# Kernel optimization log

Hardware: AMD Instinct MI355X
Metric: run time of the kernel (lower is better)

## Reference

```python
import jax, jax.numpy as jnp
import numpy as np

B, L, D = 8, 4096, 128
TEMPERATURE = 1.0


def setup_inputs() -> dict:
    key = jax.random.key(0)
    kx, kw, kb = jax.random.split(key, 3)
    x = jax.random.normal(kx, (B, L, D), dtype=jnp.float32)
    # nn.Linear(dim, dim): weight [D, D], bias [D]
    bound = 1.0 / np.sqrt(D)
    W = jax.random.uniform(kw, (D, D), minval=-bound, maxval=bound, dtype=jnp.float32)
    b = jax.random.uniform(kb, (D,), minval=-bound, maxval=bound, dtype=jnp.float32)
    return {"x": x, "W": W, "b": b}


def reference(x, W, b):
    # projected = proj(x): torch Linear is x @ W.T + b
    projected = jnp.einsum("bld,ed->ble", x, W) + b            # [B, L, D]

    # adaptive_avg_pool1d over sequence length L -> L//2 (L even => pair means)
    Bq, Lx, Dx = x.shape
    q = x.reshape(Bq, Lx // 2, 2, Dx).mean(axis=2)             # [B, L/2, D]
    q = jnp.einsum("bld,ed->ble", q, W) + b                    # [B, L/2, D]

    # pairwise squared euclidean distance via ||q||^2 + ||k||^2 - 2 q.k (GEMM form)
    q_sq = jnp.sum(q * q, axis=-1, keepdims=True)              # [B, L/2, 1]
    k_sq = jnp.sum(projected * projected, axis=-1)[:, None, :] # [B, 1, L]
    qk = jnp.einsum("bqd,bkd->bqk", q, projected)              # [B, L/2, L]
    power = jnp.maximum(q_sq + k_sq - 2.0 * qk, 0.0)
    distances = jnp.sqrt(power)
    similarities = jnp.exp(-distances * TEMPERATURE)           # [B, L/2, L]

    k = jnp.einsum("bqk,bkd->bqd", similarities, projected)    # [B, L/2, D]
    v = k
    return (q, k, v)
```

## Files before the change

### kernel.cpp

```cpp
#include <hip/hip_runtime.h>
#include <hip/hip_bf16.h>
#include <stdint.h>

#define NB 8
#define LL 4096
#define LQ 2048
#define DD 128

typedef __attribute__((ext_vector_type(8))) short short8;
typedef __attribute__((ext_vector_type(4))) short short4v;
typedef __attribute__((ext_vector_type(4))) float f4;
typedef __attribute__((ext_vector_type(2))) unsigned int u2;

typedef const __attribute__((address_space(1))) unsigned int guint_t;
typedef __attribute__((address_space(3))) unsigned int luint_t;

__device__ __forceinline__ short8 pack8(const float* v) {
    __hip_bfloat16 h[8];
    #pragma unroll
    for (int j = 0; j < 8; ++j) h[j] = __float2bfloat16(v[j]);
    return *(short8*)h;
}

__global__ __launch_bounds__(256) void projA_kernel(
    const float* __restrict__ x, const float* __restrict__ W,
    const float* __restrict__ bias,
    __hip_bfloat16* __restrict__ proj_sw, __hip_bfloat16* __restrict__ projT_sw,
    __hip_bfloat16* __restrict__ qb, float* __restrict__ qf,
    float* __restrict__ psq, float* __restrict__ qsq)
{
    __shared__ __hip_bfloat16 Wlds[128 * 128];
    __shared__ __hip_bfloat16 Tt[4][128 * 16];

    const int tid = threadIdx.x;
    const int lane = tid & 63, w = tid >> 6;
    const int lr = lane & 15, lh = lane >> 4;

    #pragma unroll
    for (int k = 0; k < 16; ++k) {
        const int f = k * 1024 + tid * 4;
        const int e = f >> 7, col = f & 127;
        f4 v = *(const f4*)&W[f];
        __hip_bfloat16 h[4];
        #pragma unroll
        for (int j = 0; j < 4; ++j) h[j] = __float2bfloat16(v[j]);
        const int byte = e * 256 + (((col * 2)) ^ ((e & 7) << 4));
        *(u2*)((char*)Wlds + byte) = *(u2*)h;
    }
    float bv[8];
    #pragma unroll
    for (int nt = 0; nt < 8; ++nt) bv[nt] = bias[nt * 16 + lr];
    __syncthreads();

    const int tile = blockIdx.x;
    const int row0 = tile * 64 + w * 16;
    const bool qmode = tile >= (NB * LL / 64);

    short8 a[4];
    if (!qmode) {
        const float* src = x + (size_t)(row0 + lr) * DD;
        #pragma unroll
        for (int ks = 0; ks < 4; ++ks) {
            float t[8];
            *(f4*)&t[0] = *(const f4*)&src[ks * 32 + lh * 8];
            *(f4*)&t[4] = *(const f4*)&src[ks * 32 + lh * 8 + 4];
            a[ks] = pack8(t);
        }
    } else {
        const int gq = row0 - NB * LL + lr;
        const int b = gq >> 11, l = gq & 2047;
        const float* s0 = x + ((size_t)b * LL + 2 * l) * DD;
        #pragma unroll
        for (int ks = 0; ks < 4; ++ks) {
            float t[8];
            f4 u0 = *(const f4*)&s0[ks * 32 + lh * 8];
            f4 u1 = *(const f4*)&s0[ks * 32 + lh * 8 + 4];
            f4 v0 = *(const f4*)&s0[DD + ks * 32 + lh * 8];
            f4 v1 = *(const f4*)&s0[DD + ks * 32 + lh * 8 + 4];
            *(f4*)&t[0] = (u0 + v0) * 0.5f;
            *(f4*)&t[4] = (u1 + v1) * 0.5f;
            a[ks] = pack8(t);
        }
    }

    f4 acc[8] = {};
    #pragma unroll
    for (int nt = 0; nt < 8; ++nt) {
        const int e = nt * 16 + lr;
        #pragma unroll
        for (int ks = 0; ks < 4; ++ks) {
            const int byte = e * 256 + ((ks * 64 + lh * 16) ^ ((lr & 7) << 4));
            short8 bk = *(const short8*)((char*)Wlds + byte);
            acc[nt] = __builtin_amdgcn_mfma_f32_16x16x32_bf16(a[ks], bk, acc[nt], 0, 0, 0);
        }
    }

    __hip_bfloat16 h[8][4];
    f4 rn = {0.f, 0.f, 0.f, 0.f};
    #pragma unroll
    for (int nt = 0; nt < 8; ++nt)
        #pragma unroll
        for (int r = 0; r < 4; ++r) {
            float v = acc[nt][r] + bv[nt];
            acc[nt][r] = v;
            h[nt][r] = __float2bfloat16(v);
            float vb = __bfloat162float(h[nt][r]);
            rn[r] += vb * vb;
        }
    #pragma unroll
    for (int m = 1; m < 16; m <<= 1) {
        #pragma unroll
        for (int r = 0; r < 4; ++r) rn[r] += __shfl_xor(rn[r], m);
    }

    if (!qmode) {
        const int gr = row0;
        #pragma unroll
        for (int nt = 0; nt < 8; ++nt)
            #pragma unroll
            for (int r = 0; r < 4; ++r) {
                const int row = gr + lh * 4 + r;
                const int byte = (nt * 32 + lr * 2) ^ (((lh * 4 + r) & 7) << 4);
                *(__hip_bfloat16*)((char*)proj_sw + (size_t)row * 256 + byte) =
                    __float2bfloat16(-2.0f * __bfloat162float(h[nt][r]));
            }
        if (lr == 0) *(f4*)&psq[gr + lh * 4] = rn;
        #pragma unroll
        for (int nt = 0; nt < 8; ++nt) {
            __hip_bfloat16 p[4] = {h[nt][0], h[nt][1], h[nt][2], h[nt][3]};
            *(u2*)((char*)&Tt[w][0] + (nt * 16 + lr) * 32 + lh * 8) = *(u2*)p;
        }
        const int b = gr >> 12, l0 = gr & 4095;
        #pragma unroll
        for (int i = 0; i < 2; ++i) {
            const int e = lane + i * 64;
            const int sw = (e & 15) << 3;
            char* rowbase = (char*)projT_sw + ((size_t)(b * DD + e)) * (LL * 2)
                          + (size_t)(l0 & ~63) * 2;
            const int ob = (l0 & 63) * 2;
            #pragma unroll
            for (int c = 0; c < 4; ++c) {
                u2 chunk = *(u2*)((char*)&Tt[w][e * 16] + c * 8);
                *(u2*)(rowbase + ((ob + c * 8) ^ sw)) = chunk;
            }
        }
    } else {
        const int gq = row0 - NB * LL;
        #pragma unroll
        for (int nt = 0; nt < 8; ++nt)
            #pragma unroll
            for (int r = 0; r < 4; ++r) {
                const size_t idx = (size_t)(gq + lh * 4 + r) * DD + nt * 16 + lr;
                qb[idx] = h[nt][r];
                qf[idx] = acc[nt][r];
            }
        if (lr == 0) *(f4*)&qsq[gq + lh * 4] = rn;
    }
}

__global__ __launch_bounds__(1024, 4) void fused_kernel(
    const __hip_bfloat16* __restrict__ proj_sw, const __hip_bfloat16* __restrict__ projT_sw,
    const __hip_bfloat16* __restrict__ qb, const float* __restrict__ psq,
    const float* __restrict__ qsq,
    float* __restrict__ pp0, float* __restrict__ pp1,
    float* __restrict__ pp2, float* __restrict__ pp3, int keys_per)
{
    __shared__ __hip_bfloat16 pbuf[2][8192];
    __shared__ __hip_bfloat16 tbuf[2][8192];
    __shared__ __align__(16) float psbuf[1024];

    const int bid = blockIdx.x;
    const int b = bid & 7;
    const int qt8 = (bid >> 3) & 7;
    const int ks = bid >> 6;
    const int tid = threadIdx.x;
    const int w = tid >> 6, lane = tid & 63;
    const int lr = lane & 15, lh = lane >> 4;

    const int qrow0 = qt8 * 256 + w * 16;
    const int key0 = ks * keys_per;
    const int ntiles = keys_per / 64;

    const char* psw = (const char*)proj_sw + (size_t)b * LL * 256;
    const char* ptbsw = (const char*)projT_sw + (size_t)b * DD * LL * 2;
    const float* psb = psq + b * LL;

    for (int i = tid; i < keys_per; i += 1024) psbuf[i] = psb[key0 + i];

    short8 aq[4];
    const __hip_bfloat16* qbase = qb + ((size_t)b * LQ + qrow0) * DD;
    #pragma unroll
    for (int kss = 0; kss < 4; ++kss)
        aq[kss] = *(const short8*)&qbase[(size_t)lr * DD + kss * 32 + lh * 8];
    const float qn = qsq[b * LQ + qrow0 + lr];

    __syncthreads();

    const char* sp = psw + (size_t)key0 * 256 + w * 1024;
    const char* st = ptbsw + (size_t)(w * 8 + (lane >> 3)) * (LL * 2)
                   + (size_t)key0 * 2 + (lane & 7) * 16;
    auto stage = [&](int buf) {
        __builtin_amdgcn_global_load_lds(
            (guint_t*)(sp + lane * 16),
            (luint_t*)&pbuf[buf][w * 512 + lane * 8], 16, 0, 0);
        __builtin_amdgcn_global_load_lds(
            (guint_t*)st,
            (luint_t*)&tbuf[buf][w * 512 + lane * 8], 16, 0, 0);
        sp += 64 * 256;
        st += 64 * 2;
    };

    stage(0);
    stage(1);

    f4 oc[8] = {};
    int p = 0;

    for (int t = 0; t < ntiles; ++t) {
        if (t + 1 < ntiles) asm volatile("s_waitcnt vmcnt(2)" ::: "memory");
        else                asm volatile("s_waitcnt vmcnt(0)" ::: "memory");
        asm volatile("s_barrier" ::: "memory");

        #pragma unroll
        for (int sub = 0; sub < 2; ++sub) {
            f4 pn0 = *(const f4*)&psbuf[t * 64 + sub * 32 + lh * 4];
            f4 pn1 = *(const f4*)&psbuf[t * 64 + sub * 32 + 16 + lh * 4];
            f4 s0, s1;
            #pragma unroll
            for (int r = 0; r < 4; ++r) {
                s0[r] = qn + pn0[r];
                s1[r] = qn + pn1[r];
            }
            __builtin_amdgcn_s_setprio(1);
            #pragma unroll
            for (int kss = 0; kss < 4; ++kss) {
                const int off = (kss * 64 + lh * 16) ^ ((lr & 7) << 4);
                short8 ak0 = *(const short8*)((const char*)pbuf[p] + (sub * 32 + lr) * 256 + off);
                short8 ak1 = *(const short8*)((const char*)pbuf[p] + (sub * 32 + 16 + lr) * 256 + off);
                s0 = __builtin_amdgcn_mfma_f32_16x16x32_bf16(ak0, aq[kss], s0, 0, 0, 0);
                s1 = __builtin_amdgcn_mfma_f32_16x16x32_bf16(ak1, aq[kss], s1, 0, 0, 0);
            }
            __builtin_amdgcn_s_setprio(0);

            alignas(16) __hip_bfloat16 hh[8];
            #pragma unroll
            for (int r = 0; r < 4; ++r) {
                float d0 = __builtin_amdgcn_sqrtf(fmaxf(s0[r], 0.0f));
                float d1 = __builtin_amdgcn_sqrtf(fmaxf(s1[r], 0.0f));
                hh[r]     = __float2bfloat16(__expf(-d0));
                hh[4 + r] = __float2bfloat16(__expf(-d1));
            }
            const short8 pa = *(short8*)hh;

            __builtin_amdgcn_s_setprio(1);
            #pragma unroll
            for (int dt = 0; dt < 8; ++dt) {
                const char* rowp = (const char*)tbuf[p] + (dt * 16 + lr) * 128;
                const int sw = lr << 3;
                union { short8 v; short4v h[2]; } u;
                u.h[0] = *(const short4v*)(rowp + ((lh * 8 + sub * 64) ^ sw));
                u.h[1] = *(const short4v*)(rowp + ((lh * 8 + 32 + sub * 64) ^ sw));
                oc[dt] = __builtin_amdgcn_mfma_f32_16x16x32_bf16(pa, u.v, oc[dt], 0, 0, 0);
            }
            __builtin_amdgcn_s_setprio(0);
        }

        asm volatile("s_barrier" ::: "memory");
        if (t + 2 < ntiles) stage(p);
        p ^= 1;
    }

    float* pb = (ks == 0) ? pp0 : (ks == 1) ? pp1 : (ks == 2) ? pp2 : pp3;
    #pragma unroll
    for (int dt = 0; dt < 8; ++dt)
        #pragma unroll
        for (int r = 0; r < 4; ++r)
            pb[((size_t)b * LQ + qrow0 + lh * 4 + r) * DD + dt * 16 + lr] = oc[dt][r];
}

__global__ __launch_bounds__(256) void reduce_kernel(
    const float* __restrict__ p0, const float* __restrict__ p1,
    const float* __restrict__ p2, const float* __restrict__ p3,
    float* __restrict__ outk, float* __restrict__ outv, int nsplit)
{
    const int b = blockIdx.x & 7;
    const size_t j = (size_t)b * (LQ * DD) + ((size_t)(blockIdx.x >> 3) * 256 + threadIdx.x) * 4;
    f4 v = *(const f4*)&p0[j] + *(const f4*)&p1[j];
    if (nsplit == 4) v += *(const f4*)&p2[j] + *(const f4*)&p3[j];
    *(f4*)&outk[j] = v;
    *(f4*)&outv[j] = v;
}

extern "C" void kernel_launch(void* const* d_in, const int* in_sizes, int n_in,
                              void* d_out, int out_size, void* d_ws, size_t ws_size,
                              hipStream_t stream) {
    const float* x = (const float*)d_in[0];
    const float* W = (const float*)d_in[1];
    const float* bias = (const float*)d_in[2];

    float* out = (float*)d_out;
    const size_t NQ = (size_t)NB * LQ * DD;
    float* qf = out;
    float* outk = out + NQ;
    float* outv = out + 2 * NQ;

    char* ws = (char*)d_ws;
    __hip_bfloat16* proj  = (__hip_bfloat16*)ws;
    __hip_bfloat16* projT = (__hip_bfloat16*)(ws + 8u * 1024 * 1024);
    __hip_bfloat16* qb    = (__hip_bfloat16*)(ws + 16u * 1024 * 1024);
    float* psq            = (float*)(ws + 20u * 1024 * 1024);
    float* qsq            = (float*)(ws + 20u * 1024 * 1024 + 256u * 1024);
    float* pw2            = (float*)(ws + 24u * 1024 * 1024);
    float* pw3            = (float*)(ws + 32u * 1024 * 1024);

    const int nsplit = (ws_size >= (40ull << 20)) ? 4 : 2;
    const int keys_per = LL / nsplit;

    hipLaunchKernelGGL(projA_kernel, dim3((NB * LL + NB * LQ) / 64), dim3(256), 0, stream,
                       x, W, bias, proj, projT, qb, qf, psq, qsq);
    hipLaunchKernelGGL(fused_kernel, dim3(64 * nsplit), dim3(1024), 0, stream,
                       proj, projT, qb, psq, qsq, outk, outv, pw2, pw3, keys_per);
    hipLaunchKernelGGL(reduce_kernel, dim3(2048), dim3(256), 0, stream,
                       outk, outv, pw2, pw3, outk, outv, nsplit);
}
```

Baseline: 78.74 us.

## Drop LDS staging in fused kernel; load key tiles directly from global

The fused distance/softmax-like kernel stops staging key and transposed-key tiles into double-buffered LDS with global_load_lds and barriers. Each wave now reads its MFMA operands directly from global memory (relying on L1/L2), and blocks shrink from 1024 to 256 threads with four times as many blocks. This removes barrier synchronisation and LDS traffic, but each wave now issues its own uncoalesced, latency-exposed global loads, and tiles are no longer shared across the 16 waves of a block.

After: 197.9 us. 2.51x slower.

```diff
diff --git a/kernel.cpp b/kernel.cpp
--- a/kernel.cpp
+++ b/kernel.cpp
@@ -11,9 +11,6 @@
 typedef __attribute__((ext_vector_type(4))) short short4v;
 typedef __attribute__((ext_vector_type(4))) float f4;
 typedef __attribute__((ext_vector_type(2))) unsigned int u2;
-
-typedef const __attribute__((address_space(1))) unsigned int guint_t;
-typedef __attribute__((address_space(3))) unsigned int luint_t;
 
 __device__ __forceinline__ short8 pack8(const float* v) {
     __hip_bfloat16 h[8];
@@ -158,34 +155,32 @@
     }
 }
 
-__global__ __launch_bounds__(1024, 4) void fused_kernel(
+__global__ __launch_bounds__(256, 4) void fused_kernel(
     const __hip_bfloat16* __restrict__ proj_sw, const __hip_bfloat16* __restrict__ projT_sw,
     const __hip_bfloat16* __restrict__ qb, const float* __restrict__ psq,
     const float* __restrict__ qsq,
     float* __restrict__ pp0, float* __restrict__ pp1,
     float* __restrict__ pp2, float* __restrict__ pp3, int keys_per)
 {
-    __shared__ __hip_bfloat16 pbuf[2][8192];
-    __shared__ __hip_bfloat16 tbuf[2][8192];
-    __shared__ __align__(16) float psbuf[1024];
+    __shared__ __align__(16) float psbuf[2048];
 
     const int bid = blockIdx.x;
     const int b = bid & 7;
-    const int qt8 = (bid >> 3) & 7;
-    const int ks = bid >> 6;
+    const int qt = (bid >> 3) & 31;
+    const int ks = bid >> 8;
     const int tid = threadIdx.x;
     const int w = tid >> 6, lane = tid & 63;
     const int lr = lane & 15, lh = lane >> 4;
 
-    const int qrow0 = qt8 * 256 + w * 16;
+    const int qrow0 = qt * 64 + w * 16;
     const int key0 = ks * keys_per;
-    const int ntiles = keys_per / 64;
+    const int niter = keys_per / 64;
 
     const char* psw = (const char*)proj_sw + (size_t)b * LL * 256;
     const char* ptbsw = (const char*)projT_sw + (size_t)b * DD * LL * 2;
     const float* psb = psq + b * LL;
 
-    for (int i = tid; i < keys_per; i += 1024) psbuf[i] = psb[key0 + i];
+    for (int i = tid; i < keys_per; i += 256) psbuf[i] = psb[key0 + i];
 
     short8 aq[4];
     const __hip_bfloat16* qbase = qb + ((size_t)b * LQ + qrow0) * DD;
@@ -196,51 +191,31 @@
 
     __syncthreads();
 
-    const char* sp = psw + (size_t)key0 * 256 + w * 1024;
-    const char* st = ptbsw + (size_t)(w * 8 + (lane >> 3)) * (LL * 2)
-                   + (size_t)key0 * 2 + (lane & 7) * 16;
-    auto stage = [&](int buf) {
-        __builtin_amdgcn_global_load_lds(
-            (guint_t*)(sp + lane * 16),
-            (luint_t*)&pbuf[buf][w * 512 + lane * 8], 16, 0, 0);
-        __builtin_amdgcn_global_load_lds(
-            (guint_t*)st,
-            (luint_t*)&tbuf[buf][w * 512 + lane * 8], 16, 0, 0);
-        sp += 64 * 256;
-        st += 64 * 2;
-    };
-
-    stage(0);
-    stage(1);
+    const char* pA = psw + (size_t)key0 * 256 + lr * 256;
+    const char* pB = ptbsw + (size_t)lr * (LL * 2) + (size_t)key0 * 2;
+    const int swB = lr << 3;
 
     f4 oc[8] = {};
-    int p = 0;
-
-    for (int t = 0; t < ntiles; ++t) {
-        if (t + 1 < ntiles) asm volatile("s_waitcnt vmcnt(2)" ::: "memory");
-        else                asm volatile("s_waitcnt vmcnt(0)" ::: "memory");
-        asm volatile("s_barrier" ::: "memory");
-
+
+    for (int it = 0; it < niter; ++it) {
         #pragma unroll
         for (int sub = 0; sub < 2; ++sub) {
-            f4 pn0 = *(const f4*)&psbuf[t * 64 + sub * 32 + lh * 4];
-            f4 pn1 = *(const f4*)&psbuf[t * 64 + sub * 32 + 16 + lh * 4];
+            f4 pn0 = *(const f4*)&psbuf[it * 64 + sub * 32 + lh * 4];
+            f4 pn1 = *(const f4*)&psbuf[it * 64 + sub * 32 + 16 + lh * 4];
             f4 s0, s1;
             #pragma unroll
             for (int r = 0; r < 4; ++r) {
                 s0[r] = qn + pn0[r];
                 s1[r] = qn + pn1[r];
             }
-            __builtin_amdgcn_s_setprio(1);
             #pragma unroll
             for (int kss = 0; kss < 4; ++kss) {
                 const int off = (kss * 64 + lh * 16) ^ ((lr & 7) << 4);
-                short8 ak0 = *(const short8*)((const char*)pbuf[p] + (sub * 32 + lr) * 256 + off);
-                short8 ak1 = *(const short8*)((const char*)pbuf[p] + (sub * 32 + 16 + lr) * 256 + off);
+                short8 ak0 = *(const short8*)(pA + (sub * 32) * 256 + off);
+                short8 ak1 = *(const short8*)(pA + (sub * 32 + 16) * 256 + off);
                 s0 = __builtin_amdgcn_mfma_f32_16x16x32_bf16(ak0, aq[kss], s0, 0, 0, 0);
                 s1 = __builtin_amdgcn_mfma_f32_16x16x32_bf16(ak1, aq[kss], s1, 0, 0, 0);
             }
-            __builtin_amdgcn_s_setprio(0);
 
             alignas(16) __hip_bfloat16 hh[8];
             #pragma unroll
@@ -252,22 +227,17 @@
             }
             const short8 pa = *(short8*)hh;
 
-            __builtin_amdgcn_s_setprio(1);
             #pragma unroll
             for (int dt = 0; dt < 8; ++dt) {
-                const char* rowp = (const char*)tbuf[p] + (dt * 16 + lr) * 128;
-                const int sw = lr << 3;
+                const char* rowp = pB + (size_t)(dt * 16) * (LL * 2);
                 union { short8 v; short4v h[2]; } u;
-                u.h[0] = *(const short4v*)(rowp + ((lh * 8 + sub * 64) ^ sw));
-                u.h[1] = *(const short4v*)(rowp + ((lh * 8 + 32 + sub * 64) ^ sw));
+                u.h[0] = *(const short4v*)(rowp + ((lh * 8 + sub * 64) ^ swB));
+                u.h[1] = *(const short4v*)(rowp + ((lh * 8 + 32 + sub * 64) ^ swB));
                 oc[dt] = __builtin_amdgcn_mfma_f32_16x16x32_bf16(pa, u.v, oc[dt], 0, 0, 0);
             }
-            __builtin_amdgcn_s_setprio(0);
-        }
-
-        asm volatile("s_barrier" ::: "memory");
-        if (t + 2 < ntiles) stage(p);
-        p ^= 1;
+        }
+        pA += 64 * 256;
+        pB += 64 * 2;
     }
 
     float* pb = (ks == 0) ? pp0 : (ks == 1) ? pp1 : (ks == 2) ? pp2 : pp3;
@@ -318,7 +288,7 @@
 
     hipLaunchKernelGGL(projA_kernel, dim3((NB * LL + NB * LQ) / 64), dim3(256), 0, stream,
                        x, W, bias, proj, projT, qb, qf, psq, qsq);
-    hipLaunchKernelGGL(fused_kernel, dim3(64 * nsplit), dim3(1024), 0, stream,
+    hipLaunchKernelGGL(fused_kernel, dim3(256 * nsplit), dim3(256), 0, stream,
                        proj, projT, qb, psq, qsq, outk, outv, pw2, pw3, keys_per);
     hipLaunchKernelGGL(reduce_kernel, dim3(2048), dim3(256), 0, stream,
                        outk, outv, pw2, pw3, outk, outv, nsplit);
```
